# Performance work log

Hardware: AMD Instinct MI355X
Metric: run time of the kernel (lower is better)

Reference implementation:

```python
import jax, jax.numpy as jnp
import numpy as np

B, T, C, H = 8, 1024, 768, 12
D = C // H  # head_dim = 64

def _rope_tables(seq_len, d, base=10000.0):
    inv_freq = 1.0 / (base ** (jnp.arange(0, d, 2, dtype=jnp.float32) / d))  # [d/2]
    freqs = jnp.outer(jnp.arange(seq_len, dtype=jnp.float32), inv_freq)      # [T, d/2]
    return jnp.cos(freqs), jnp.sin(freqs)

def _apply_rotary(x, cos, sin):
    # x: [B,T,H,D]; cos/sin: [1,T,1,D/2]
    d = x.shape[-1] // 2
    x1, x2 = x[..., :d], x[..., d:]
    return jnp.concatenate([x1 * cos + x2 * sin, -x1 * sin + x2 * cos], axis=-1)

def setup_inputs() -> dict:
    key = jax.random.key(0)
    k1, k2, k3 = jax.random.split(key, 3)
    x = jax.random.normal(k1, (B, T, C), dtype=jnp.float32)
    w_qkv = jax.random.normal(k2, (3 * C, C), dtype=jnp.float32) * (C ** -0.5)
    w_proj = jax.random.normal(k3, (C, C), dtype=jnp.float32) * (C ** -0.5)
    return {"x": x, "w_qkv": w_qkv, "w_proj": w_proj}

def reference(x, w_qkv, w_proj):
    Bb, Tt, Cc = x.shape
    qkv = x @ w_qkv.T                                   # [B,T,3C]
    q, k, v = jnp.split(qkv, 3, axis=2)
    q = q.reshape(Bb, Tt, H, D)
    k = k.reshape(Bb, Tt, H, D)
    v = v.reshape(Bb, Tt, H, D)
    cos, sin = _rope_tables(Tt, D)
    cos = cos[None, :, None, :]
    sin = sin[None, :, None, :]
    q = _apply_rotary(q, cos, sin)
    k = _apply_rotary(k, cos, sin)
    scale = 1.0 / jnp.sqrt(jnp.float32(D))
    scores = jnp.einsum('bthd,bshd->bhts', q, k) * scale  # [B,H,T,T]
    causal = jnp.tril(jnp.ones((Tt, Tt), dtype=bool))
    scores = jnp.where(causal[None, None], scores, jnp.finfo(scores.dtype).min)
    p = jax.nn.softmax(scores, axis=-1)
    y = jnp.einsum('bhts,bshd->bthd', p, v).reshape(Bb, Tt, Cc)
    return y @ w_proj.T
```

## Files before the change

### kernel.cpp

```cpp
#include <hip/hip_runtime.h>
#include <hip/hip_bf16.h>

#define Bb 8
#define Tt 1024
#define Cc 768
#define Hh 12
#define Dd 64
#define M_ROWS (Bb * Tt)
#define QKV_N (3 * Cc)

typedef __attribute__((ext_vector_type(8))) short s16x8;
typedef __attribute__((ext_vector_type(4))) short s16x4;
typedef __attribute__((ext_vector_type(4))) float f32x4;

#define AS1 __attribute__((address_space(1)))
#define AS3 __attribute__((address_space(3)))

static __device__ __forceinline__ short f2bf(float f) {
    union { float f; unsigned u; } v; v.f = f;
    unsigned r = (v.u + 0x7fffu + ((v.u >> 16) & 1u)) >> 16;
    return (short)r;
}

static __device__ __forceinline__ void cast8(const float* __restrict__ in,
                                             short* __restrict__ out, int i) {
    const float4 a = ((const float4*)in)[i * 2];
    const float4 b = ((const float4*)in)[i * 2 + 1];
    s16x8 f;
    f[0] = f2bf(a.x); f[1] = f2bf(a.y); f[2] = f2bf(a.z); f[3] = f2bf(a.w);
    f[4] = f2bf(b.x); f[5] = f2bf(b.y); f[6] = f2bf(b.z); f[7] = f2bf(b.w);
    ((s16x8*)out)[i] = f;
}

#define S1 (M_ROWS * Cc / 8)
#define S2 (QKV_N * Cc / 8)
#define S3 (Cc * Cc / 8)
#define SROPE (Tt * 32)
#define PREP_THREADS (S1 + S2 + S3 + SROPE)

__global__ __launch_bounds__(256) void prep_kernel(const float* __restrict__ x,
                                                   const float* __restrict__ wqkv,
                                                   const float* __restrict__ wproj,
                                                   short* __restrict__ xb,
                                                   short* __restrict__ wqkvb,
                                                   short* __restrict__ wprojb,
                                                   float2* __restrict__ cs) {
    int idx = blockIdx.x * blockDim.x + threadIdx.x;
    if (idx < S1) { cast8(x, xb, idx); return; }
    idx -= S1;
    if (idx < S2) { cast8(wqkv, wqkvb, idx); return; }
    idx -= S2;
    if (idx < S3) { cast8(wproj, wprojb, idx); return; }
    idx -= S3;
    {
        int t = idx >> 5, i = idx & 31;
        float inv_freq = exp2f(-0.41524101186092037f * (float)i);
        float fr = (float)t * inv_freq;
        float2 v; v.x = cosf(fr); v.y = sinf(fr);
        cs[idx] = v;
    }
}

template <int MODE>
__global__ __launch_bounds__(256) void gemm_nt_mfma(const short* __restrict__ A,
                                                    const short* __restrict__ B,
                                                    void* __restrict__ Cout,
                                                    const float2* __restrict__ cs,
                                                    int M, int N, int K, int nblocks) {
    __shared__ short As[2][128 * 32];
    __shared__ short Bs[2][128 * 32];

    const int wave = threadIdx.x >> 6;
    const int lane = threadIdx.x & 63;
    const int l16  = lane & 15;
    const int quad = lane >> 4;
    const int wm = (wave >> 1) * 64;
    const int wn = (wave & 1) * 64;

    const int mb8  = (M >> 7) >> 3;
    const int xcd  = blockIdx.x & 7;
    const int slot = blockIdx.x >> 3;
    const int bm = (xcd * mb8 + slot / nblocks) * 128;
    const int bn = (slot % nblocks) * 128;

    f32x4 acc[4][4] = {};

    auto stage = [&](int k0, int buf) {
#pragma unroll
        for (int j = 0; j < 2; j++) {
            const int D = (j * 4 + wave) * 64 + lane;
            const int G = D >> 3;
            const int s = (G << 3) | ((D & 7) ^ (G & 7));
            const int m  = s >> 2;
            const int c4 = (s & 3) * 8;
            __builtin_amdgcn_global_load_lds(
                (const AS1 unsigned*)(A + (size_t)(bm + m) * K + k0 + c4),
                (AS3 unsigned*)&As[buf][(j * 4 + wave) * 512], 16, 0, 0);
            __builtin_amdgcn_global_load_lds(
                (const AS1 unsigned*)(B + (size_t)(bn + m) * K + k0 + c4),
                (AS3 unsigned*)&Bs[buf][(j * 4 + wave) * 512], 16, 0, 0);
        }
    };

    const int nIter = K >> 5;
    stage(0, 0);
    for (int kt = 0; kt < nIter; kt++) {
        const int buf = kt & 1;
        __syncthreads();
        if (kt + 1 < nIter) stage((kt + 1) << 5, buf ^ 1);

        s16x8 af[4], bfr[4];
#pragma unroll
        for (int mt = 0; mt < 4; mt++) {
            const int m = wm + mt * 16 + l16;
            const int d = (4 * (m & 1) + quad) ^ ((m >> 1) & 7);
            af[mt] = *(const s16x8*)&As[buf][(m >> 1) * 64 + d * 8];
        }
#pragma unroll
        for (int nt = 0; nt < 4; nt++) {
            const int n = wn + nt * 16 + l16;
            const int d = (4 * (n & 1) + quad) ^ ((n >> 1) & 7);
            bfr[nt] = *(const s16x8*)&Bs[buf][(n >> 1) * 64 + d * 8];
        }
#pragma unroll
        for (int mt = 0; mt < 4; mt++)
#pragma unroll
            for (int nt = 0; nt < 4; nt++)
                acc[mt][nt] = __builtin_amdgcn_mfma_f32_16x16x32_bf16(
                    af[mt], bfr[nt], acc[mt][nt], 0, 0, 0);
    }

    if constexpr (MODE == 0) {
#pragma unroll
        for (int mt = 0; mt < 4; mt++)
#pragma unroll
            for (int r = 0; r < 4; r++) {
                const size_t row = bm + wm + mt * 16 + quad * 4 + r;
#pragma unroll
                for (int nt = 0; nt < 4; nt++)
                    ((float*)Cout)[row * N + bn + wn + nt * 16 + l16] = acc[mt][nt][r];
            }
    } else {
        const bool is_v = (bn >= 2 * Cc);
        if (is_v) {
#pragma unroll
            for (int mt = 0; mt < 4; mt++)
#pragma unroll
                for (int r = 0; r < 4; r++) {
                    const size_t row = bm + wm + mt * 16 + quad * 4 + r;
#pragma unroll
                    for (int nt = 0; nt < 4; nt++)
                        ((short*)Cout)[row * N + bn + wn + nt * 16 + l16] = f2bf(acc[mt][nt][r]);
                }
        } else {
            const float scale = (bn < Cc) ? 0.125f : 1.0f;
#pragma unroll
            for (int mt = 0; mt < 4; mt++) {
#pragma unroll
                for (int r = 0; r < 4; r++) {
                    const int row = bm + wm + mt * 16 + quad * 4 + r;
                    const int t = row & (Tt - 1);
                    const float2 c0 = cs[t * 32 + l16];
                    const float2 c1 = cs[t * 32 + 16 + l16];
                    const float x0 = acc[mt][0][r], x1 = acc[mt][1][r];
                    const float x2 = acc[mt][2][r], x3 = acc[mt][3][r];
                    short* cp = (short*)Cout + (size_t)row * N + bn + wn;
                    cp[l16]      = f2bf((x0 * c0.x + x2 * c0.y) * scale);
                    cp[16 + l16] = f2bf((x1 * c1.x + x3 * c1.y) * scale);
                    cp[32 + l16] = f2bf((-x0 * c0.y + x2 * c0.x) * scale);
                    cp[48 + l16] = f2bf((-x1 * c1.y + x3 * c1.x) * scale);
                }
            }
        }
    }
}

#define KSP 72
#define VSP 72
#define PP  76

__global__ __launch_bounds__(256) void flash_attn(const short* __restrict__ qkv,
                                                  short* __restrict__ y) {
    __shared__ short Ks[2][64 * KSP];
    __shared__ short Vs[2][Dd * VSP];
    __shared__ short Ps[4][16 * PP];

    const int wave = threadIdx.x >> 6;
    const int lane = threadIdx.x & 63;
    const int l16  = lane & 15;
    const int quad = lane >> 4;

    const int pair = blockIdx.x / 96;
    const int bh   = blockIdx.x % 96;
    const int h = bh % Hh;
    const int b = bh / Hh;
    const int qa_blk = pair;
    const int qb_blk = 15 - pair;
    const int q0a = qa_blk * 64 + wave * 16;
    const int q0b = qb_blk * 64 + wave * 16;

    s16x8 qfa[2], qfb[2];
    {
        const short* qpa = qkv + (size_t)(b * Tt + q0a + l16) * QKV_N + h * Dd + quad * 8;
        const short* qpb = qkv + (size_t)(b * Tt + q0b + l16) * QKV_N + h * Dd + quad * 8;
        qfa[0] = *(const s16x8*)qpa;  qfa[1] = *(const s16x8*)(qpa + 32);
        qfb[0] = *(const s16x8*)qpb;  qfb[1] = *(const s16x8*)(qpb + 32);
    }

    f32x4 oa[4] = {}, ob[4] = {};
    float la[4] = {0.f, 0.f, 0.f, 0.f}, lb[4] = {0.f, 0.f, 0.f, 0.f};

    short* pw = &Ps[wave][0];

    const int krow = threadIdx.x >> 2;
    const int kd0  = (threadIdx.x & 3) * 16;
    const int key2 = (threadIdx.x & 31) * 2;
    const int dv0  = (threadIdx.x >> 5) * 8;

    s16x8 pk0, pk1, pv0, pv1;
    auto load_tile = [&](int kbase) {
        const short* kp = qkv + (size_t)(b * Tt + kbase + krow) * QKV_N + Cc + h * Dd + kd0;
        pk0 = *(const s16x8*)kp;
        pk1 = *(const s16x8*)(kp + 8);
        const short* vp = qkv + (size_t)(b * Tt + kbase + key2) * QKV_N + 2 * Cc + h * Dd + dv0;
        pv0 = *(const s16x8*)vp;
        pv1 = *(const s16x8*)(vp + QKV_N);
    };
    auto store_tile = [&](int buf) {
        *(s16x8*)&Ks[buf][krow * KSP + kd0]     = pk0;
        *(s16x8*)&Ks[buf][krow * KSP + kd0 + 8] = pk1;
#pragma unroll
        for (int j = 0; j < 8; j++) {
            ushort2 w; w.x = (unsigned short)pv0[j]; w.y = (unsigned short)pv1[j];
            *(ushort2*)&Vs[buf][(dv0 + j) * VSP + key2] = w;
        }
    };

    auto process = [&](int buf, int q0, const s16x8* qf, f32x4* o, float* l_r,
                       int kbase, bool masked) {
        f32x4 sv[4];
#pragma unroll
        for (int g = 0; g < 4; g++) {
            s16x8 kf0 = *(const s16x8*)&Ks[buf][(g * 16 + l16) * KSP + quad * 8];
            s16x8 kf1 = *(const s16x8*)&Ks[buf][(g * 16 + l16) * KSP + 32 + quad * 8];
            f32x4 z = {};
            z = __builtin_amdgcn_mfma_f32_16x16x32_bf16(qf[0], kf0, z, 0, 0, 0);
            z = __builtin_amdgcn_mfma_f32_16x16x32_bf16(qf[1], kf1, z, 0, 0, 0);
            sv[g] = z;
        }
#pragma unroll
        for (int r = 0; r < 4; r++) {
            const int qg = q0 + quad * 4 + r;
            float rs = 0.f;
#pragma unroll
            for (int g = 0; g < 4; g++) {
                float p = __expf(sv[g][r]);
                if (masked) p = (kbase + g * 16 + l16 <= qg) ? p : 0.0f;
                rs += p;
                pw[(quad * 4 + r) * PP + g * 16 + l16] = f2bf(p);
            }
            l_r[r] += rs;
        }
#pragma unroll
        for (int c = 0; c < 2; c++) {
            s16x4 plo = *(const s16x4*)&pw[l16 * PP + c * 32 + quad * 8];
            s16x4 phi = *(const s16x4*)&pw[l16 * PP + c * 32 + quad * 8 + 4];
            s16x8 pa = __builtin_shufflevector(plo, phi, 0, 1, 2, 3, 4, 5, 6, 7);
#pragma unroll
            for (int nc = 0; nc < 4; nc++) {
                s16x8 vb = *(const s16x8*)&Vs[buf][(nc * 16 + l16) * VSP + c * 32 + quad * 8];
                o[nc] = __builtin_amdgcn_mfma_f32_16x16x32_bf16(pa, vb, o[nc], 0, 0, 0);
            }
        }
    };

    load_tile(0);
    store_tile(0);
    for (int kt = 0; kt <= qb_blk; kt++) {
        __syncthreads();
        const int nb = (kt < qb_blk) ? (kt + 1) * 64 : qb_blk * 64;
        load_tile(nb);
        const int buf = kt & 1;
        const int kbase = kt * 64;
        process(buf, q0b, qfb, ob, lb, kbase, kt == qb_blk);
        if (kt <= qa_blk)
            process(buf, q0a, qfa, oa, la, kbase, kt == qa_blk);
        store_tile(buf ^ 1);
    }

#pragma unroll
    for (int r = 0; r < 4; r++) {
        float sa = la[r], sb = lb[r];
#pragma unroll
        for (int off = 1; off < 16; off <<= 1) {
            sa += __shfl_xor(sa, off, 64);
            sb += __shfl_xor(sb, off, 64);
        }
        const float inva = 1.0f / sa;
        const float invb = 1.0f / sb;
        short* ypa = y + (size_t)(b * Tt + q0a + quad * 4 + r) * Cc + h * Dd;
        short* ypb = y + (size_t)(b * Tt + q0b + quad * 4 + r) * Cc + h * Dd;
#pragma unroll
        for (int nc = 0; nc < 4; nc++) {
            ypa[nc * 16 + l16] = f2bf(oa[nc][r] * inva);
            ypb[nc * 16 + l16] = f2bf(ob[nc][r] * invb);
        }
    }
}

extern "C" void kernel_launch(void* const* d_in, const int* in_sizes, int n_in,
                              void* d_out, int out_size, void* d_ws, size_t ws_size,
                              hipStream_t stream) {
    const float* x      = (const float*)d_in[0];
    const float* w_qkv  = (const float*)d_in[1];
    const float* w_proj = (const float*)d_in[2];
    float* out = (float*)d_out;

    float2* cs    = (float2*)d_ws;
    short* xb     = (short*)(cs + Tt * 32);
    short* wqkvb  = xb + (size_t)M_ROWS * Cc;
    short* wprojb = wqkvb + (size_t)QKV_N * Cc;
    short* qkvb   = wprojb + (size_t)Cc * Cc;
    short* yb     = qkvb + (size_t)M_ROWS * QKV_N;

    prep_kernel<<<PREP_THREADS / 256, 256, 0, stream>>>(
        x, w_qkv, w_proj, xb, wqkvb, wprojb, cs);

    gemm_nt_mfma<1><<<(QKV_N / 128) * (M_ROWS / 128), 256, 0, stream>>>(
        xb, wqkvb, qkvb, cs, M_ROWS, QKV_N, Cc, QKV_N / 128);

    flash_attn<<<96 * 8, 256, 0, stream>>>(qkvb, yb);

    gemm_nt_mfma<0><<<(Cc / 128) * (M_ROWS / 128), 256, 0, stream>>>(
        yb, wprojb, out, nullptr, M_ROWS, Cc, Cc, Cc / 128);
}
```

Before: 185.1 us.

## Retile GEMM to 128xTN blocks with 32-row waves and templated N tile

```diff
diff --git a/kernel.cpp b/kernel.cpp
--- a/kernel.cpp
+++ b/kernel.cpp
@@ -61,44 +61,49 @@
     }
 }
 
-template <int MODE>
-__global__ __launch_bounds__(256) void gemm_nt_mfma(const short* __restrict__ A,
-                                                    const short* __restrict__ B,
-                                                    void* __restrict__ Cout,
-                                                    const float2* __restrict__ cs,
-                                                    int M, int N, int K, int nblocks) {
+template <int MODE, int TN>
+__global__ __launch_bounds__(256, 3) void gemm_nt_mfma(const short* __restrict__ A,
+                                                       const short* __restrict__ B,
+                                                       void* __restrict__ Cout,
+                                                       const float2* __restrict__ cs,
+                                                       int M, int N, int K, int nblocks) {
     __shared__ short As[2][128 * 32];
-    __shared__ short Bs[2][128 * 32];
+    __shared__ short Bs[2][TN * 32];
+    constexpr int NT = TN / 16;
 
     const int wave = threadIdx.x >> 6;
     const int lane = threadIdx.x & 63;
     const int l16  = lane & 15;
     const int quad = lane >> 4;
-    const int wm = (wave >> 1) * 64;
-    const int wn = (wave & 1) * 64;
 
     const int mb8  = (M >> 7) >> 3;
     const int xcd  = blockIdx.x & 7;
     const int slot = blockIdx.x >> 3;
     const int bm = (xcd * mb8 + slot / nblocks) * 128;
-    const int bn = (slot % nblocks) * 128;
-
-    f32x4 acc[4][4] = {};
+    const int bn = (slot % nblocks) * TN;
+
+    f32x4 acc[2][NT] = {};
 
     auto stage = [&](int k0, int buf) {
 #pragma unroll
         for (int j = 0; j < 2; j++) {
-            const int D = (j * 4 + wave) * 64 + lane;
+            const int D = j * 256 + wave * 64 + lane;
             const int G = D >> 3;
             const int s = (G << 3) | ((D & 7) ^ (G & 7));
-            const int m  = s >> 2;
-            const int c4 = (s & 3) * 8;
+            const int m = s >> 2, c4 = (s & 3) * 8;
             __builtin_amdgcn_global_load_lds(
                 (const AS1 unsigned*)(A + (size_t)(bm + m) * K + k0 + c4),
-                (AS3 unsigned*)&As[buf][(j * 4 + wave) * 512], 16, 0, 0);
+                (AS3 unsigned*)&As[buf][(j * 256 + wave * 64) * 8], 16, 0, 0);
+        }
+#pragma unroll
+        for (int j = 0; j < TN / 64; j++) {
+            const int D = j * 256 + wave * 64 + lane;
+            const int G = D >> 3;
+            const int s = (G << 3) | ((D & 7) ^ (G & 7));
+            const int m = s >> 2, c4 = (s & 3) * 8;
             __builtin_amdgcn_global_load_lds(
                 (const AS1 unsigned*)(B + (size_t)(bn + m) * K + k0 + c4),
-                (AS3 unsigned*)&Bs[buf][(j * 4 + wave) * 512], 16, 0, 0);
+                (AS3 unsigned*)&Bs[buf][(j * 256 + wave * 64) * 8], 16, 0, 0);
         }
     };
 
@@ -109,66 +114,67 @@
         __syncthreads();
         if (kt + 1 < nIter) stage((kt + 1) << 5, buf ^ 1);
 
-        s16x8 af[4], bfr[4];
-#pragma unroll
-        for (int mt = 0; mt < 4; mt++) {
-            const int m = wm + mt * 16 + l16;
-            const int d = (4 * (m & 1) + quad) ^ ((m >> 1) & 7);
+        s16x8 af[2];
+#pragma unroll
+        for (int mt = 0; mt < 2; mt++) {
+            const int m = wave * 32 + mt * 16 + l16;
+            const int d = ((m & 1) * 4 + quad) ^ ((m >> 1) & 7);
             af[mt] = *(const s16x8*)&As[buf][(m >> 1) * 64 + d * 8];
         }
 #pragma unroll
-        for (int nt = 0; nt < 4; nt++) {
-            const int n = wn + nt * 16 + l16;
-            const int d = (4 * (n & 1) + quad) ^ ((n >> 1) & 7);
-            bfr[nt] = *(const s16x8*)&Bs[buf][(n >> 1) * 64 + d * 8];
-        }
-#pragma unroll
-        for (int mt = 0; mt < 4; mt++)
-#pragma unroll
-            for (int nt = 0; nt < 4; nt++)
-                acc[mt][nt] = __builtin_amdgcn_mfma_f32_16x16x32_bf16(
-                    af[mt], bfr[nt], acc[mt][nt], 0, 0, 0);
+        for (int nt = 0; nt < NT; nt++) {
+            const int n = nt * 16 + l16;
+            const int d = ((n & 1) * 4 + quad) ^ ((n >> 1) & 7);
+            s16x8 bf = *(const s16x8*)&Bs[buf][(n >> 1) * 64 + d * 8];
+            acc[0][nt] = __builtin_amdgcn_mfma_f32_16x16x32_bf16(af[0], bf, acc[0][nt], 0, 0, 0);
+            acc[1][nt] = __builtin_amdgcn_mfma_f32_16x16x32_bf16(af[1], bf, acc[1][nt], 0, 0, 0);
+        }
     }
 
     if constexpr (MODE == 0) {
 #pragma unroll
-        for (int mt = 0; mt < 4; mt++)
+        for (int mt = 0; mt < 2; mt++)
 #pragma unroll
             for (int r = 0; r < 4; r++) {
-                const size_t row = bm + wm + mt * 16 + quad * 4 + r;
-#pragma unroll
-                for (int nt = 0; nt < 4; nt++)
-                    ((float*)Cout)[row * N + bn + wn + nt * 16 + l16] = acc[mt][nt][r];
+                const size_t row = bm + wave * 32 + mt * 16 + quad * 4 + r;
+#pragma unroll
+                for (int nt = 0; nt < NT; nt++)
+                    ((float*)Cout)[row * N + bn + nt * 16 + l16] = acc[mt][nt][r];
             }
     } else {
         const bool is_v = (bn >= 2 * Cc);
         if (is_v) {
 #pragma unroll
-            for (int mt = 0; mt < 4; mt++)
+            for (int mt = 0; mt < 2; mt++)
 #pragma unroll
                 for (int r = 0; r < 4; r++) {
-                    const size_t row = bm + wm + mt * 16 + quad * 4 + r;
-#pragma unroll
-                    for (int nt = 0; nt < 4; nt++)
-                        ((short*)Cout)[row * N + bn + wn + nt * 16 + l16] = f2bf(acc[mt][nt][r]);
+                    const size_t row = bm + wave * 32 + mt * 16 + quad * 4 + r;
+#pragma unroll
+                    for (int nt = 0; nt < NT; nt++)
+                        ((short*)Cout)[row * N + bn + nt * 16 + l16] = f2bf(acc[mt][nt][r]);
                 }
         } else {
             const float scale = (bn < Cc) ? 0.125f : 1.0f;
 #pragma unroll
-            for (int mt = 0; mt < 4; mt++) {
+            for (int mt = 0; mt < 2; mt++) {
 #pragma unroll
                 for (int r = 0; r < 4; r++) {
-                    const int row = bm + wm + mt * 16 + quad * 4 + r;
+                    const int row = bm + wave * 32 + mt * 16 + quad * 4 + r;
                     const int t = row & (Tt - 1);
                     const float2 c0 = cs[t * 32 + l16];
                     const float2 c1 = cs[t * 32 + 16 + l16];
-                    const float x0 = acc[mt][0][r], x1 = acc[mt][1][r];
-                    const float x2 = acc[mt][2][r], x3 = acc[mt][3][r];
-                    short* cp = (short*)Cout + (size_t)row * N + bn + wn;
-                    cp[l16]      = f2bf((x0 * c0.x + x2 * c0.y) * scale);
-                    cp[16 + l16] = f2bf((x1 * c1.x + x3 * c1.y) * scale);
-                    cp[32 + l16] = f2bf((-x0 * c0.y + x2 * c0.x) * scale);
-                    cp[48 + l16] = f2bf((-x1 * c1.y + x3 * c1.x) * scale);
+#pragma unroll
+                    for (int hh = 0; hh < TN / 64; hh++) {
+                        const float x0 = acc[mt][hh * 4 + 0][r];
+                        const float x1 = acc[mt][hh * 4 + 1][r];
+                        const float x2 = acc[mt][hh * 4 + 2][r];
+                        const float x3 = acc[mt][hh * 4 + 3][r];
+                        short* cp = (short*)Cout + (size_t)row * N + bn + hh * 64;
+                        cp[l16]      = f2bf((x0 * c0.x + x2 * c0.y) * scale);
+                        cp[16 + l16] = f2bf((x1 * c1.x + x3 * c1.y) * scale);
+                        cp[32 + l16] = f2bf((-x0 * c0.y + x2 * c0.x) * scale);
+                        cp[48 + l16] = f2bf((-x1 * c1.y + x3 * c1.x) * scale);
+                    }
                 }
             }
         }
@@ -326,11 +332,11 @@
     prep_kernel<<<PREP_THREADS / 256, 256, 0, stream>>>(
         x, w_qkv, w_proj, xb, wqkvb, wprojb, cs);
 
-    gemm_nt_mfma<1><<<(QKV_N / 128) * (M_ROWS / 128), 256, 0, stream>>>(
-        xb, wqkvb, qkvb, cs, M_ROWS, QKV_N, Cc, QKV_N / 128);
+    gemm_nt_mfma<1, 192><<<768, 256, 0, stream>>>(
+        xb, wqkvb, qkvb, cs, M_ROWS, QKV_N, Cc, QKV_N / 192);
 
     flash_attn<<<96 * 8, 256, 0, stream>>>(qkvb, yb);
 
-    gemm_nt_mfma<0><<<(Cc / 128) * (M_ROWS / 128), 256, 0, stream>>>(
+    gemm_nt_mfma<0, 128><<<384, 256, 0, stream>>>(
         yb, wprojb, out, nullptr, M_ROWS, Cc, Cc, Cc / 128);
 }
```

Result: faster. 175.2 us (-5.3%).
